# Optimization experiments

Measured on AMD Instinct MI355X. Metric: run time of the kernel, lower is better.

## Reference

```python
import jax, jax.numpy as jnp
import numpy as np

WS = 7   # window size
NH = 6   # num heads

def _ln(x, g, b, eps=1e-5):
    m = x.mean(-1, keepdims=True)
    v = jnp.var(x, axis=-1, keepdims=True)
    return (x - m) * jax.lax.rsqrt(v + eps) * g + b

def setup_inputs() -> dict:
    key = jax.random.key(0)
    ks = jax.random.split(key, 12)
    B, H, W, C = 32, 56, 56, 192
    hid = int(C * 2.0)
    def n(k, shape, s=0.02):
        return jax.random.normal(k, shape, jnp.float32) * s
    return {
        "x": jax.random.normal(ks[0], (B, H * W, C), jnp.float32),
        "H": H, "W": W,
        "ln1_g": jnp.ones((C,), jnp.float32), "ln1_b": jnp.zeros((C,), jnp.float32),
        "qkv_w": n(ks[1], (3 * C, C)), "qkv_b": jnp.zeros((3 * C,), jnp.float32),
        "proj_w": n(ks[2], (C, C)), "proj_b": jnp.zeros((C,), jnp.float32),
        "dw_w": n(ks[3], (C, 1, 3, 3)),          # depthwise 3x3, groups=C
        "pw_w": n(ks[4], (C, C)),                 # pointwise 1x1 conv (no bias)
        "gate_w": n(ks[5], (C, C)), "gate_b": jnp.zeros((C,), jnp.float32),
        "temp_w": n(ks[6], (C, C)), "temp_b": jnp.zeros((C,), jnp.float32),
        "spec_w": n(ks[7], (C, C)), "spec_b": jnp.zeros((C,), jnp.float32),
        "fuse_w": n(ks[8], (C, C)),                # fuse 1x1 conv (no bias)
        "ln2_g": jnp.ones((C,), jnp.float32), "ln2_b": jnp.zeros((C,), jnp.float32),
        "mlp1_w": n(ks[9], (hid, C)), "mlp1_b": jnp.zeros((hid,), jnp.float32),
        "mlp2_w": n(ks[10], (C, hid)), "mlp2_b": jnp.zeros((C,), jnp.float32),
    }

def reference(x, H, W, ln1_g, ln1_b, qkv_w, qkv_b, proj_w, proj_b, dw_w, pw_w,
              gate_w, gate_b, temp_w, temp_b, spec_w, spec_b, fuse_w,
              ln2_g, ln2_b, mlp1_w, mlp1_b, mlp2_w, mlp2_b):
    B, L, C = x.shape
    hd = C // NH
    scale = hd ** -0.5
    shortcut = x
    xn = _ln(x, ln1_g, ln1_b).reshape(B, H, W, C)
    # pad to multiple of window size (no-op when divisible)
    pad_b = (-H) % WS
    pad_r = (-W) % WS
    xp = jnp.pad(xn, ((0, 0), (0, pad_b), (0, pad_r), (0, 0)))
    Hp, Wp = H + pad_b, W + pad_r
    # window partition -> [B*nW, N, C]
    xw = xp.reshape(B, Hp // WS, WS, Wp // WS, WS, C).transpose(0, 1, 3, 2, 4, 5).reshape(-1, WS * WS, C)
    qkv = xw @ qkv_w.T + qkv_b
    q, k, v = [t.reshape(-1, WS * WS, NH, hd).transpose(0, 2, 1, 3) for t in jnp.split(qkv, 3, axis=-1)]
    attn = jax.nn.softmax(jnp.einsum('whnd,whmd->whnm', q * scale, k), axis=-1)
    aw = jnp.einsum('whnm,whmd->whnd', attn, v).transpose(0, 2, 1, 3).reshape(-1, WS * WS, C)
    aw = aw @ proj_w.T + proj_b
    # window reverse -> [B, Hp, Wp, C]
    xr = aw.reshape(B, Hp // WS, Wp // WS, WS, WS, C).transpose(0, 1, 3, 2, 4, 5).reshape(B, Hp, Wp, C)
    x_attn = xr[:, :H, :W, :].transpose(0, 3, 1, 2)     # [B,C,H,W]
    x_conv = xn.transpose(0, 3, 1, 2)                    # [B,C,H,W]
    # local_conv: depthwise 3x3 -> GELU -> pointwise 1x1
    ld = jax.lax.conv_general_dilated(x_conv, dw_w, (1, 1), 'SAME',
                                      feature_group_count=C,
                                      dimension_numbers=('NCHW', 'OIHW', 'NCHW'))
    ld = jnp.einsum('oc,bchw->bohw', pw_w, jax.nn.gelu(ld, approximate=False))
    # global gate: GAP -> linear -> sigmoid
    gate = jax.nn.sigmoid(x_conv.mean((2, 3)) @ gate_w.T + gate_b)[:, :, None, None]
    xf = x_attn + ld + x_conv * gate
    # spectral-temporal attention (outer product of two softmaxes, scale=2.0)
    a_t = jax.nn.softmax(jnp.einsum('oc,bcw->bow', temp_w, xf.mean(2)) + temp_b[None, :, None], axis=-1)
    a_s = jax.nn.softmax(jnp.einsum('oc,bch->boh', spec_w, xf.mean(3)) + spec_b[None, :, None], axis=-1)
    xf = xf * (a_s[:, :, :, None] * a_t[:, :, None, :]) * 2.0
    xf = jnp.einsum('oc,bchw->bohw', fuse_w, xf)         # fuse 1x1 conv
    x = shortcut + xf.transpose(0, 2, 3, 1).reshape(B, H * W, C)
    # MLP with pre-norm residual (1x1 conv expand == linear, then fc)
    h = _ln(x, ln2_g, ln2_b)
    h = jax.nn.gelu(h @ mlp1_w.T + mlp1_b, approximate=False)
    x = x + (h @ mlp2_w.T + mlp2_b)
    return x
```

## Files before the change

### kernel.cpp

```cpp
#include <hip/hip_runtime.h>
#include <hip/hip_bf16.h>

typedef __hip_bfloat16 bf16;

#define BB 32
#define HH 56
#define WW 56
#define CC 192
#define LL 3136
#define MM (BB*LL)
#define C3 576
#define HIDN 384
#define NHEAD 6
#define HD 32
#define NWIN 2048

typedef short short8 __attribute__((ext_vector_type(8)));
typedef float f32x4 __attribute__((ext_vector_type(4)));

__device__ __forceinline__ float us2f(unsigned short u) {
    union { unsigned int i; float f; } v; v.i = ((unsigned int)u) << 16; return v.f;
}
__device__ __forceinline__ float b2f(bf16 h) { return __bfloat162float(h); }
__device__ __forceinline__ bf16 f2b(float f) { return __float2bfloat16(f); }
__device__ __forceinline__ short f2bs(float f) { bf16 h = f2b(f); return *reinterpret_cast<short*>(&h); }
__device__ __forceinline__ unsigned pk2(float a, float b) {
    return (unsigned)(unsigned short)f2bs(a) | ((unsigned)(unsigned short)f2bs(b) << 16);
}
__device__ __forceinline__ float ldv(const bf16* p) { return b2f(*p); }
__device__ __forceinline__ float ldv(const float* p) { return *p; }
__device__ __forceinline__ void stv(bf16* p, float v) { *p = f2b(v); }
__device__ __forceinline__ void stv(float* p, float v) { *p = v; }
__device__ __forceinline__ float gelu_exact(float x) {
    return 0.5f * x * (1.0f + erff(x * 0.70710678118654752f));
}
__device__ __forceinline__ void async_lds16(const void* g, void* l) {
    __builtin_amdgcn_global_load_lds(
        (const __attribute__((address_space(1))) void*)g,
        (__attribute__((address_space(3))) void*)l, 16, 0, 0);
}

__global__ __launch_bounds__(256)
void cvt8_kernel(const float* __restrict__ s0, bf16* __restrict__ d0, int n0,
                 const float* __restrict__ s1, bf16* __restrict__ d1, int n1,
                 const float* __restrict__ s2, bf16* __restrict__ d2, int n2,
                 const float* __restrict__ s3, bf16* __restrict__ d3, int n3,
                 const float* __restrict__ s4, bf16* __restrict__ d4, int n4,
                 const float* __restrict__ s5, bf16* __restrict__ d5, int n5,
                 const float* __restrict__ s6, bf16* __restrict__ d6, int n6,
                 const float* __restrict__ s7, bf16* __restrict__ d7, int n7)
{
    int i = blockIdx.x * 256 + threadIdx.x;
    if (i < n0) { d0[i] = f2b(s0[i]); return; } i -= n0;
    if (i < n1) { d1[i] = f2b(s1[i]); return; } i -= n1;
    if (i < n2) { d2[i] = f2b(s2[i]); return; } i -= n2;
    if (i < n3) { d3[i] = f2b(s3[i]); return; } i -= n3;
    if (i < n4) { d4[i] = f2b(s4[i]); return; } i -= n4;
    if (i < n5) { d5[i] = f2b(s5[i]); return; } i -= n5;
    if (i < n6) { d6[i] = f2b(s6[i]); return; } i -= n6;
    if (i < n7) { d7[i] = f2b(s7[i]); }
}

template<typename IT>
__global__ __launch_bounds__(256)
void ln_kernel(const IT* __restrict__ in, const float* __restrict__ g,
               const float* __restrict__ bvec, bf16* __restrict__ out,
               bf16* __restrict__ xcopy)
{
    int wid = threadIdx.x >> 6, lane = threadIdx.x & 63;
    int row = blockIdx.x * 4 + wid;
    const IT* p = in + (size_t)row * CC;
    float x0 = ldv(p + lane);
    float x1 = ldv(p + lane + 64);
    float x2 = ldv(p + lane + 128);
    float s  = x0 + x1 + x2;
    float sq = x0*x0 + x1*x1 + x2*x2;
    #pragma unroll
    for (int o = 32; o > 0; o >>= 1) {
        s  += __shfl_xor(s,  o, 64);
        sq += __shfl_xor(sq, o, 64);
    }
    float mean = s * (1.0f / CC);
    float var  = sq * (1.0f / CC) - mean * mean;
    float inv  = rsqrtf(fmaxf(var, 0.0f) + 1e-5f);
    bf16* q = out + (size_t)row * CC;
    q[lane]       = f2b((x0 - mean) * inv * g[lane]       + bvec[lane]);
    q[lane + 64]  = f2b((x1 - mean) * inv * g[lane + 64]  + bvec[lane + 64]);
    q[lane + 128] = f2b((x2 - mean) * inv * g[lane + 128] + bvec[lane + 128]);
    if (xcopy) {
        bf16* xq = xcopy + (size_t)row * CC;
        xq[lane]       = f2b(x0);
        xq[lane + 64]  = f2b(x1);
        xq[lane + 128] = f2b(x2);
    }
}

template<int EPI, bool RESID, int NN, int KK, typename RT, typename OT>
__global__ __launch_bounds__(256)
void mfma_gemm(const bf16* __restrict__ A, const bf16* __restrict__ W,
               const float* __restrict__ bias, const RT* __restrict__ resid,
               OT* __restrict__ out,
               const bf16* __restrict__ xn2, const float* __restrict__ gate)
{
    __shared__ __align__(16) short Smem[128 * 64 + 64 * 64];
    short* As = Smem;
    short* Bs = Smem + 128 * 64;
    const int t    = threadIdx.x;
    const int lane = t & 63;
    const int w    = t >> 6;
    const int nx   = gridDim.x;
    const int nwg  = gridDim.x * gridDim.y;
    int hw  = blockIdx.y * nx + blockIdx.x;
    int wid = (nwg & 7) ? hw : ((hw & 7) * (nwg >> 3) + (hw >> 3));
    const int m0   = (wid / nx) * 128;
    const int n0   = (wid % nx) * 64;
    const int lr   = lane & 15;
    const int lg   = lane >> 4;

    f32x4 acc[2][4];
    #pragma unroll
    for (int i = 0; i < 2; ++i)
        #pragma unroll
        for (int j = 0; j < 4; ++j)
            acc[i][j] = (f32x4){0.f, 0.f, 0.f, 0.f};

    for (int k0 = 0; k0 < KK; k0 += 64) {
        const bf16* Ab = A + (size_t)m0 * KK + k0;
        const bf16* Wb = W + (size_t)n0 * KK + k0;
        #pragma unroll
        for (int li = 0; li < 4; ++li) {
            int chunk = li * 256 + t;
            int r = chunk >> 3, c = chunk & 7;
            int cs = c ^ (r & 7);
            async_lds16(Ab + (size_t)r * KK + (cs << 3),
                        &As[(li * 256 + w * 64) << 3]);
        }
        #pragma unroll
        for (int li = 0; li < 2; ++li) {
            int chunk = li * 256 + t;
            int r = chunk >> 3, c = chunk & 7;
            int cs = c ^ (r & 7);
            async_lds16(Wb + (size_t)r * KK + (cs << 3),
                        &Bs[(li * 256 + w * 64) << 3]);
        }
        __syncthreads();
        #pragma unroll
        for (int kf = 0; kf < 2; ++kf) {
            short8 a_[2], b_[4];
            #pragma unroll
            for (int mi = 0; mi < 2; ++mi) {
                int row = (w << 5) + (mi << 4) + lr;
                a_[mi] = *reinterpret_cast<const short8*>(
                    &As[(row << 6) + ((((kf << 2) + lg) ^ (row & 7)) << 3)]);
            }
            #pragma unroll
            for (int ni = 0; ni < 4; ++ni) {
                int rn = (ni << 4) + lr;
                b_[ni] = *reinterpret_cast<const short8*>(
                    &Bs[(rn << 6) + ((((kf << 2) + lg) ^ (rn & 7)) << 3)]);
            }
            #pragma unroll
            for (int mi = 0; mi < 2; ++mi)
                #pragma unroll
                for (int ni = 0; ni < 4; ++ni)
                    acc[mi][ni] = __builtin_amdgcn_mfma_f32_16x16x32_bf16(
                        a_[mi], b_[ni], acc[mi][ni], 0, 0, 0);
        }
        __syncthreads();
    }

    if constexpr (sizeof(OT) == 2) {
        short* cs = Smem + w * 3072;
        #pragma unroll
        for (int mi = 0; mi < 2; ++mi) {
            #pragma unroll
            for (int ni = 0; ni < 4; ++ni) {
                int col = n0 + (ni << 4) + lr;
                float bv = bias ? bias[col] : 0.f;
                #pragma unroll
                for (int r = 0; r < 4; ++r) {
                    int row = m0 + (w << 5) + (mi << 4) + (lg << 2) + r;
                    float c = acc[mi][ni][r] + bv;
                    if (EPI == 1) c = gelu_exact(c);
                    if (EPI == 2) {
                        int bidx = row / LL;
                        c += ldv(resid + (size_t)row * NN + col)
                           + b2f(xn2[(size_t)row * NN + col]) * gate[bidx * CC + col];
                    }
                    if (RESID) c += ldv(resid + (size_t)row * NN + col);
                    cs[((mi << 4) + (lg << 2) + r) * 72 + (ni << 4) + lr] = f2bs(c);
                }
            }
        }
        #pragma unroll
        for (int pass = 0; pass < 4; ++pass) {
            int r8 = (lane >> 3) + (pass << 3);
            int c8 = lane & 7;
            uint4 v = *reinterpret_cast<const uint4*>(&cs[r8 * 72 + (c8 << 3)]);
            *reinterpret_cast<uint4*>((bf16*)out + (size_t)(m0 + (w << 5) + r8) * NN
                                      + n0 + (c8 << 3)) = v;
        }
    } else {
        #pragma unroll
        for (int mi = 0; mi < 2; ++mi) {
            #pragma unroll
            for (int ni = 0; ni < 4; ++ni) {
                int col = n0 + (ni << 4) + lr;
                float bv = bias ? bias[col] : 0.f;
                #pragma unroll
                for (int r = 0; r < 4; ++r) {
                    int row = m0 + (w << 5) + (mi << 4) + (lg << 2) + r;
                    float c = acc[mi][ni][r] + bv;
                    if (EPI == 1) c = gelu_exact(c);
                    if (EPI == 2) {
                        int bidx = row / LL;
                        c += ldv(resid + (size_t)row * NN + col)
                           + b2f(xn2[(size_t)row * NN + col]) * gate[bidx * CC + col];
                    }
                    if (RESID) c += ldv(resid + (size_t)row * NN + col);
                    stv(out + (size_t)row * NN + col, c);
                }
            }
        }
    }
}

__global__ __launch_bounds__(256)
void winattn_kernel(const bf16* __restrict__ qkv, bf16* __restrict__ aw)
{
    __shared__ __align__(16) short Buf[4][2560];

    const int w  = threadIdx.x >> 6;
    const int t  = threadIdx.x & 63;
    const int p  = blockIdx.x * 4 + w;
    const int wi = p / 6;
    const int head = p - wi * 6;
    const int b  = wi >> 6;
    const int wr = wi & 63;
    const int wy = wr >> 3, wx = wr & 7;
    const int lc = t & 15;
    const int lg = t >> 4;
    const float scale = 0.1767766952966369f;
    const bf16* qbase = qkv + (size_t)b * LL * C3 + head * HD;
    short* buf = Buf[w];

    #pragma unroll
    for (int e = t; e < 512; e += 64) {
        int d = e >> 4, k = 48 + (e & 15);
        buf[(d << 6) + (((k >> 3) ^ (d & 7)) << 3) + (k & 7)] = 0;
    }
    for (int e = t; e < 196; e += 64) {
        int tok = e >> 2, part = e & 3;
        int iy = tok / 7, ix = tok - iy * 7;
        size_t l = (size_t)(wy * 7 + iy) * 56 + wx * 7 + ix;
        uint4 pv = *reinterpret_cast<const uint4*>(qbase + l * C3 + 384 + (part << 3));
        unsigned short uv[8];
        *reinterpret_cast<uint4*>(uv) = pv;
        #pragma unroll
        for (int jj = 0; jj < 8; ++jj) {
            int d = (part << 3) + jj;
            buf[(d << 6) + (((tok >> 3) ^ (d & 7)) << 3) + (tok & 7)] = (short)uv[jj];
        }
    }

    const short8 zero8 = {0, 0, 0, 0, 0, 0, 0, 0};
    short8 ka[4], qb[4];
    #pragma unroll
    for (int mi = 0; mi < 4; ++mi) {
        int key = (mi << 4) + lc;
        ka[mi] = zero8;
        if (key < 49) {
            int iy = key / 7, ix = key - iy * 7;
            size_t l = (size_t)(wy * 7 + iy) * 56 + wx * 7 + ix;
            ka[mi] = *reinterpret_cast<const short8*>(qbase + l * C3 + 192 + (lg << 3));
        }
    }
    #pragma unroll
    for (int nj = 0; nj < 4; ++nj) {
        int tok = (nj << 4) + lc;
        qb[nj] = zero8;
        if (tok < 49) {
            int iy = tok / 7, ix = tok - iy * 7;
            size_t l = (size_t)(wy * 7 + iy) * 56 + wx * 7 + ix;
            qb[nj] = *reinterpret_cast<const short8*>(qbase + l * C3 + (lg << 3));
        }
    }

    f32x4 acc[4][4];
    #pragma unroll
    for (int i = 0; i < 4; ++i)
        #pragma unroll
        for (int j = 0; j < 4; ++j)
            acc[i][j] = (f32x4){0.f, 0.f, 0.f, 0.f};
    #pragma unroll
    for (int mi = 0; mi < 4; ++mi)
        #pragma unroll
        for (int nj = 0; nj < 4; ++nj)
            acc[mi][nj] = __builtin_amdgcn_mfma_f32_16x16x32_bf16(
                ka[mi], qb[nj], acc[mi][nj], 0, 0, 0);

    float rinv[4];
    #pragma unroll
    for (int nj = 0; nj < 4; ++nj) {
        float mx = acc[0][nj][0];
        #pragma unroll
        for (int mi = 0; mi < 3; ++mi)
            #pragma unroll
            for (int r = 0; r < 4; ++r)
                mx = fmaxf(mx, acc[mi][nj][r]);
        float v48 = (lg == 0) ? acc[3][nj][0] : -1e30f;
        mx = fmaxf(mx, v48);
        mx = fmaxf(mx, __shfl_xor(mx, 16, 64));
        mx = fmaxf(mx, __shfl_xor(mx, 32, 64));
        float sm = 0.f;
        #pragma unroll
        for (int mi = 0; mi < 3; ++mi)
            #pragma unroll
            for (int r = 0; r < 4; ++r) {
                float e = __expf(scale * (acc[mi][nj][r] - mx));
                acc[mi][nj][r] = e;
                sm += e;
            }
        float e48 = (lg == 0) ? __expf(scale * (acc[3][nj][0] - mx)) : 0.f;
        acc[3][nj][0] = e48; sm += e48;
        acc[3][nj][1] = 0.f; acc[3][nj][2] = 0.f; acc[3][nj][3] = 0.f;
        sm += __shfl_xor(sm, 16, 64);
        sm += __shfl_xor(sm, 32, 64);
        rinv[nj] = 1.0f / sm;
    }

    f32x4 acc2[2][4];
    #pragma unroll
    for (int i = 0; i < 2; ++i)
        #pragma unroll
        for (int j = 0; j < 4; ++j)
            acc2[i][j] = (f32x4){0.f, 0.f, 0.f, 0.f};
    const int src0 = ((lg & 1) << 5) + lc;
    const int src1 = src0 + 16;
    const bool hi = (lg >> 1) != 0;
    #pragma unroll
    for (int kf = 0; kf < 2; ++kf) {
        short8 av[2];
        #pragma unroll
        for (int mi2 = 0; mi2 < 2; ++mi2) {
            int d = (mi2 << 4) + lc;
            av[mi2] = *reinterpret_cast<const short8*>(
                &buf[(d << 6) + ((((kf << 2) + lg) ^ (d & 7)) << 3)]);
        }
        #pragma unroll
        for (int nj = 0; nj < 4; ++nj) {
            unsigned A0 = pk2(acc[2*kf][nj][0],   acc[2*kf][nj][1]);
            unsigned A1 = pk2(acc[2*kf][nj][2],   acc[2*kf][nj][3]);
            unsigned B0 = pk2(acc[2*kf+1][nj][0], acc[2*kf+1][nj][1]);
            unsigned B1 = pk2(acc[2*kf+1][nj][2], acc[2*kf+1][nj][3]);
            unsigned xa0 = __shfl(A0, src0, 64), xa1 = __shfl(A1, src0, 64);
            unsigned xa2 = __shfl(A0, src1, 64), xa3 = __shfl(A1, src1, 64);
            unsigned xb0 = __shfl(B0, src0, 64), xb1 = __shfl(B1, src0, 64);
            unsigned xb2 = __shfl(B0, src1, 64), xb3 = __shfl(B1, src1, 64);
            union { unsigned u[4]; short8 s; } ub;
            ub.u[0] = hi ? xb0 : xa0;
            ub.u[1] = hi ? xb1 : xa1;
            ub.u[2] = hi ? xb2 : xa2;
            ub.u[3] = hi ? xb3 : xa3;
            #pragma unroll
            for (int mi2 = 0; mi2 < 2; ++mi2)
                acc2[mi2][nj] = __builtin_amdgcn_mfma_f32_16x16x32_bf16(
                    av[mi2], ub.s, acc2[mi2][nj], 0, 0, 0);
        }
    }

    #pragma unroll
    for (int mi2 = 0; mi2 < 2; ++mi2)
        #pragma unroll
        for (int nj = 0; nj < 4; ++nj) {
            int tokrow = (nj << 4) + lc;
            #pragma unroll
            for (int r = 0; r < 4; ++r) {
                int d = (mi2 << 4) + (lg << 2) + r;
                buf[tokrow * 40 + d] = f2bs(acc2[mi2][nj][r] * rinv[nj]);
            }
        }
    for (int e = t; e < 196; e += 64) {
        int tok = e >> 2, part = e & 3;
        int iy = tok / 7, ix = tok - iy * 7;
        size_t l = (size_t)(wy * 7 + iy) * 56 + wx * 7 + ix;
        *reinterpret_cast<uint4*>(aw + ((size_t)b * LL + l) * CC + head * HD + (part << 3)) =
            *reinterpret_cast<const uint4*>(&buf[tok * 40 + (part << 3)]);
    }
}

__global__ __launch_bounds__(256)
void dwconv_kernel(const bf16* __restrict__ xn, const float* __restrict__ w,
                   bf16* __restrict__ out)
{
    __shared__ float wl[9 * 288];
    const int t = threadIdx.x;
    for (int i = t; i < CC * 9; i += 256) {
        int c = i / 9, k = i - c * 9;
        wl[k * 288 + (c >> 3) * 12 + (c & 7)] = w[i];
    }
    __syncthreads();
    int e = blockIdx.x * 256 + t;
    int cg = e % 24;
    int pix = e / 24;
    int w_ = pix % WW;
    int t2 = pix / WW;
    int h_ = t2 % HH;
    int b  = t2 / HH;
    float acc[8] = {0.f,0.f,0.f,0.f,0.f,0.f,0.f,0.f};
    const bf16* rowbase = xn + ((size_t)b * HH * WW) * CC + (size_t)cg * 8;
    #pragma unroll
    for (int ky = 0; ky < 3; ++ky) {
        int hy = h_ + ky - 1;
        if (hy < 0 || hy >= HH) continue;
        #pragma unroll
        for (int kx = 0; kx < 3; ++kx) {
            int wx_ = w_ + kx - 1;
            if (wx_ < 0 || wx_ >= WW) continue;
            int k = ky * 3 + kx;
            const float4* wp = reinterpret_cast<const float4*>(&wl[k * 288 + cg * 12]);
            float4 w0 = wp[0];
            float4 w1 = wp[1];
            unsigned short u[8];
            *reinterpret_cast<uint4*>(u) = *reinterpret_cast<const uint4*>(
                rowbase + ((size_t)hy * WW + wx_) * CC);
            acc[0] += us2f(u[0]) * w0.x;
            acc[1] += us2f(u[1]) * w0.y;
            acc[2] += us2f(u[2]) * w0.z;
            acc[3] += us2f(u[3]) * w0.w;
            acc[4] += us2f(u[4]) * w1.x;
            acc[5] += us2f(u[5]) * w1.y;
            acc[6] += us2f(u[6]) * w1.z;
            acc[7] += us2f(u[7]) * w1.w;
        }
    }
    bf16 o8[8];
    #pragma unroll
    for (int j = 0; j < 8; ++j) o8[j] = f2b(gelu_exact(acc[j]));
    *reinterpret_cast<uint4*>(out + (size_t)e * 8) = *reinterpret_cast<uint4*>(o8);
}

__global__ __launch_bounds__(192)
void colsum_kernel(const bf16* __restrict__ xn, float* __restrict__ colsum)
{
    int b = blockIdx.y, g = blockIdx.x, c = threadIdx.x;
    float acc = 0.f;
    int l0 = g * 196;
    for (int l = l0; l < l0 + 196; ++l)
        acc += b2f(xn[((size_t)b * LL + l) * CC + c]);
    atomicAdd(&colsum[b * CC + c], acc);
}

__global__ __launch_bounds__(192)
void gate_kernel(const float* __restrict__ colsum, const float* __restrict__ gw,
                 const float* __restrict__ gb, float* __restrict__ gate)
{
    __shared__ float cm[CC];
    int b = blockIdx.x, o = threadIdx.x;
    cm[o] = colsum[b * CC + o] * (1.0f / LL);
    __syncthreads();
    float acc = gb[o];
    for (int c = 0; c < CC; ++c) acc += gw[o * CC + c] * cm[c];
    gate[b * CC + o] = 1.0f / (1.0f + expf(-acc));
}

__global__ __launch_bounds__(256)
void means_kernel(const bf16* __restrict__ xf, bf16* __restrict__ mh,
                  bf16* __restrict__ mw)
{
    int e = blockIdx.x * 256 + threadIdx.x;
    const int NHALF = BB * WW * 24;
    if (e < NHALF) {
        int cg = e % 24, c0 = cg << 3;
        int w_ = (e / 24) % WW;
        int b  = e / (24 * WW);
        float s[8] = {0.f,0.f,0.f,0.f,0.f,0.f,0.f,0.f};
        const bf16* base = xf + ((size_t)b * HH * WW + w_) * CC + c0;
        for (int h_ = 0; h_ < HH; ++h_) {
            unsigned short u[8];
            *reinterpret_cast<uint4*>(u) = *reinterpret_cast<const uint4*>(base + (size_t)h_ * WW * CC);
            #pragma unroll
            for (int j = 0; j < 8; ++j) s[j] += us2f(u[j]);
        }
        bf16 o8[8];
        #pragma unroll
        for (int j = 0; j < 8; ++j) o8[j] = f2b(s[j] * (1.0f / HH));
        *reinterpret_cast<uint4*>(mh + ((size_t)b * WW + w_) * CC + c0) =
            *reinterpret_cast<uint4*>(o8);
    } else {
        e -= NHALF;
        int cg = e % 24, c0 = cg << 3;
        int h_ = (e / 24) % HH;
        int b  = e / (24 * HH);
        float s[8] = {0.f,0.f,0.f,0.f,0.f,0.f,0.f,0.f};
        const bf16* base = xf + ((size_t)b * HH + h_) * WW * CC + c0;
        for (int w_ = 0; w_ < WW; ++w_) {
            unsigned short u[8];
            *reinterpret_cast<uint4*>(u) = *reinterpret_cast<const uint4*>(base + (size_t)w_ * CC);
            #pragma unroll
            for (int j = 0; j < 8; ++j) s[j] += us2f(u[j]);
        }
        bf16 o8[8];
        #pragma unroll
        for (int j = 0; j < 8; ++j) o8[j] = f2b(s[j] * (1.0f / WW));
        *reinterpret_cast<uint4*>(mw + ((size_t)b * HH + h_) * CC + c0) =
            *reinterpret_cast<uint4*>(o8);
    }
}

__global__ __launch_bounds__(256)
void axmfma_kernel(const bf16* __restrict__ mh, const bf16* __restrict__ wt,
                   float* __restrict__ at,
                   const bf16* __restrict__ mw, const bf16* __restrict__ ws,
                   float* __restrict__ as_)
{
    const int b = blockIdx.x;
    const bf16* mean; const bf16* wmat; float* out;
    if (blockIdx.y == 0) { mean = mh; wmat = wt; out = at; }
    else                 { mean = mw; wmat = ws; out = as_; }
    const int w  = threadIdx.x >> 6;
    const int t  = threadIdx.x & 63;
    const int lc = t & 15, lg = t >> 4;
    const bf16* mb = mean + (size_t)b * 56 * CC;
    const short8 zero8 = {0, 0, 0, 0, 0, 0, 0, 0};

    f32x4 acc[3][4];
    #pragma unroll
    for (int i = 0; i < 3; ++i)
        #pragma unroll
        for (int j = 0; j < 4; ++j)
            acc[i][j] = (f32x4){0.f, 0.f, 0.f, 0.f};

    #pragma unroll
    for (int kf = 0; kf < 6; ++kf) {
        short8 a_[3], b_[4];
        #pragma unroll
        for (int mi = 0; mi < 3; ++mi) {
            int o = ((w * 3 + mi) << 4) + lc;
            a_[mi] = *reinterpret_cast<const short8*>(wmat + (size_t)o * CC + (kf << 5) + (lg << 3));
        }
        #pragma unroll
        for (int ni = 0; ni < 4; ++ni) {
            int pos = (ni << 4) + lc;
            b_[ni] = (pos < 56)
                ? *reinterpret_cast<const short8*>(mb + (size_t)pos * CC + (kf << 5) + (lg << 3))
                : zero8;
        }
        #pragma unroll
        for (int mi = 0; mi < 3; ++mi)
            #pragma unroll
            for (int ni = 0; ni < 4; ++ni)
                acc[mi][ni] = __builtin_amdgcn_mfma_f32_16x16x32_bf16(
                    a_[mi], b_[ni], acc[mi][ni], 0, 0, 0);
    }

    #pragma unroll
    for (int mi = 0; mi < 3; ++mi) {
        #pragma unroll
        for (int r = 0; r < 4; ++r) {
            float mx = -1e30f;
            #pragma unroll
            for (int ni = 0; ni < 4; ++ni) {
                float v = acc[mi][ni][r];
                if (ni == 3 && lc >= 8) v = -1e30f;
                mx = fmaxf(mx, v);
            }
            mx = fmaxf(mx, __shfl_xor(mx, 1, 64));
            mx = fmaxf(mx, __shfl_xor(mx, 2, 64));
            mx = fmaxf(mx, __shfl_xor(mx, 4, 64));
            mx = fmaxf(mx, __shfl_xor(mx, 8, 64));
            float e[4];
            float sm = 0.f;
            #pragma unroll
            for (int ni = 0; ni < 4; ++ni) {
                e[ni] = (ni == 3 && lc >= 8) ? 0.f : __expf(acc[mi][ni][r] - mx);
                sm += e[ni];
            }
            sm += __shfl_xor(sm, 1, 64);
            sm += __shfl_xor(sm, 2, 64);
            sm += __shfl_xor(sm, 4, 64);
            sm += __shfl_xor(sm, 8, 64);
            float inv = 1.0f / sm;
            int o = ((w * 3 + mi) << 4) + (lg << 2) + r;
            #pragma unroll
            for (int ni = 0; ni < 4; ++ni) {
                int pos = (ni << 4) + lc;
                if (pos < 56)
                    out[((size_t)b * 56 + pos) * CC + o] = e[ni] * inv;
            }
        }
    }
}

__global__ __launch_bounds__(256)
void modulate_kernel(const bf16* __restrict__ xf, const float* __restrict__ a_s,
                     const float* __restrict__ a_t, bf16* __restrict__ xf2)
{
    int e = blockIdx.x * 256 + threadIdx.x;
    int cg = e % 24, c0 = cg << 3;
    int pix = e / 24;
    int w_ = pix % WW;
    int t2 = pix / WW;
    int h_ = t2 % HH;
    int b  = t2 / HH;
    unsigned short u[8];
    size_t base = (size_t)e * 8;
    *reinterpret_cast<uint4*>(u) = *reinterpret_cast<const uint4*>(xf + base);
    const float4* sp = reinterpret_cast<const float4*>(a_s + ((size_t)b * 56 + h_) * CC + c0);
    const float4* tp = reinterpret_cast<const float4*>(a_t + ((size_t)b * 56 + w_) * CC + c0);
    float4 s0 = sp[0], s1 = sp[1];
    float4 t0 = tp[0], t1 = tp[1];
    float ss[8] = {s0.x, s0.y, s0.z, s0.w, s1.x, s1.y, s1.z, s1.w};
    float tt[8] = {t0.x, t0.y, t0.z, t0.w, t1.x, t1.y, t1.z, t1.w};
    bf16 o8[8];
    #pragma unroll
    for (int j = 0; j < 8; ++j)
        o8[j] = f2b(us2f(u[j]) * ss[j] * tt[j] * 2.0f);
    *reinterpret_cast<uint4*>(xf2 + base) = *reinterpret_cast<uint4*>(o8);
}

extern "C" void kernel_launch(void* const* d_in, const int* in_sizes, int n_in,
                              void* d_out, int out_size, void* d_ws, size_t ws_size,
                              hipStream_t stream)
{
    const float* x      = (const float*)d_in[0];
    const float* ln1_g  = (const float*)d_in[3];
    const float* ln1_b  = (const float*)d_in[4];
    const float* qkv_w  = (const float*)d_in[5];
    const float* qkv_b  = (const float*)d_in[6];
    const float* proj_w = (const float*)d_in[7];
    const float* proj_b = (const float*)d_in[8];
    const float* dw_w   = (const float*)d_in[9];
    const float* pw_w   = (const float*)d_in[10];
    const float* gate_w = (const float*)d_in[11];
    const float* gate_b = (const float*)d_in[12];
    const float* temp_w = (const float*)d_in[13];
    const float* spec_w = (const float*)d_in[15];
    const float* fuse_w = (const float*)d_in[17];
    const float* ln2_g  = (const float*)d_in[18];
    const float* ln2_b  = (const float*)d_in[19];
    const float* mlp1_w = (const float*)d_in[20];
    const float* mlp1_b = (const float*)d_in[21];
    const float* mlp2_w = (const float*)d_in[22];
    const float* mlp2_b = (const float*)d_in[23];
    float* out = (float*)d_out;

    const size_t SLOT = (size_t)MM * CC * sizeof(bf16);
    char* ws = (char*)d_ws;

    bf16* s_xn    = (bf16*)(ws);
    bf16* s_qkv   = (bf16*)(ws + SLOT);
    bf16* s_aw    = (bf16*)(ws + 4 * SLOT);
    bf16* s_xattn = (bf16*)(ws + SLOT);
    bf16* s_dwg   = (bf16*)(ws + 2 * SLOT);
    bf16* s_xf    = (bf16*)(ws + 4 * SLOT);
    bf16* s_xf2   = (bf16*)(ws + 3 * SLOT);
    bf16* s_x2    = (bf16*)(ws);
    bf16* s_hn    = (bf16*)(ws + 2 * SLOT);
    bf16* s_h1    = (bf16*)(ws + 3 * SLOT);

    float* colsum  = (float*)(ws + 5 * SLOT);
    float* gatebuf = colsum + BB * CC;
    bf16*  mean_h  = (bf16*)(gatebuf + BB * CC);
    bf16*  mean_w  = mean_h + (size_t)BB * 56 * CC;
    float* a_t     = (float*)(mean_w + (size_t)BB * 56 * CC);
    float* a_s     = a_t + (size_t)BB * CC * 56;
    bf16* wb_qkv  = (bf16*)(a_s + (size_t)BB * CC * 56);
    bf16* wb_proj = wb_qkv  + C3 * CC;
    bf16* wb_pw   = wb_proj + CC * CC;
    bf16* wb_fuse = wb_pw   + CC * CC;
    bf16* wb_mlp1 = wb_fuse + CC * CC;
    bf16* wb_mlp2 = wb_mlp1 + HIDN * CC;
    bf16* wb_temp = wb_mlp2 + CC * HIDN;
    bf16* wb_spec = wb_temp + CC * CC;
    char* after_w = (char*)(wb_spec + CC * CC);
    size_t total_need = after_w - ws;
    if (ws_size < total_need) return;
    bf16* s_xb = (bf16*)after_w;
    bool have_xb = (ws_size >= total_need + SLOT);

    const int VEC_BLOCKS = MM * 24 / 256;
    const int CVT_N0 = C3 * CC, CVT_N1 = CC * CC, CVT_N4 = HIDN * CC;
    const int CVT_TOTAL = CVT_N0 + 5 * CVT_N1 + 2 * CVT_N4;

    cvt8_kernel<<<(CVT_TOTAL + 255) / 256, 256, 0, stream>>>(
        qkv_w, wb_qkv, CVT_N0, proj_w, wb_proj, CVT_N1, pw_w, wb_pw, CVT_N1,
        fuse_w, wb_fuse, CVT_N1, mlp1_w, wb_mlp1, CVT_N4, mlp2_w, wb_mlp2, CVT_N4,
        temp_w, wb_temp, CVT_N1, spec_w, wb_spec, CVT_N1);

    ln_kernel<float><<<MM / 4, 256, 0, stream>>>(x, ln1_g, ln1_b, s_xn,
                                                 have_xb ? s_xb : nullptr);
    mfma_gemm<0, false, C3, CC, bf16, bf16><<<dim3(C3 / 64, MM / 128), 256, 0, stream>>>(
        s_xn, wb_qkv, qkv_b, (const bf16*)nullptr, s_qkv, nullptr, nullptr);
    winattn_kernel<<<NWIN * NHEAD / 4, 256, 0, stream>>>(s_qkv, s_aw);
    mfma_gemm<0, false, CC, CC, bf16, bf16><<<dim3(CC / 64, MM / 128), 256, 0, stream>>>(
        s_aw, wb_proj, proj_b, (const bf16*)nullptr, s_xattn, nullptr, nullptr);
    dwconv_kernel<<<VEC_BLOCKS, 256, 0, stream>>>(s_xn, dw_w, s_dwg);
    hipMemsetAsync(colsum, 0, BB * CC * sizeof(float), stream);
    colsum_kernel<<<dim3(16, BB), 192, 0, stream>>>(s_xn, colsum);
    gate_kernel<<<BB, 192, 0, stream>>>(colsum, gate_w, gate_b, gatebuf);
    mfma_gemm<2, false, CC, CC, bf16, bf16><<<dim3(CC / 64, MM / 128), 256, 0, stream>>>(
        s_dwg, wb_pw, (const float*)nullptr, s_xattn, s_xf, s_xn, gatebuf);
    means_kernel<<<(2 * BB * WW * 24) / 256, 256, 0, stream>>>(s_xf, mean_h, mean_w);
    axmfma_kernel<<<dim3(BB, 2), 256, 0, stream>>>(
        mean_h, wb_temp, a_t, mean_w, wb_spec, a_s);
    modulate_kernel<<<VEC_BLOCKS, 256, 0, stream>>>(s_xf, a_s, a_t, s_xf2);
    if (have_xb)
        mfma_gemm<0, true, CC, CC, bf16, bf16><<<dim3(CC / 64, MM / 128), 256, 0, stream>>>(
            s_xf2, wb_fuse, (const float*)nullptr, s_xb, s_x2, nullptr, nullptr);
    else
        mfma_gemm<0, true, CC, CC, float, bf16><<<dim3(CC / 64, MM / 128), 256, 0, stream>>>(
            s_xf2, wb_fuse, (const float*)nullptr, x, s_x2, nullptr, nullptr);
    ln_kernel<bf16><<<MM / 4, 256, 0, stream>>>(s_x2, ln2_g, ln2_b, s_hn, nullptr);
    mfma_gemm<1, false, HIDN, CC, bf16, bf16><<<dim3(HIDN / 64, MM / 128), 256, 0, stream>>>(
        s_hn, wb_mlp1, mlp1_b, (const bf16*)nullptr, s_h1, nullptr, nullptr);
    mfma_gemm<0, true, CC, HIDN, bf16, float><<<dim3(CC / 64, MM / 128), 256, 0, stream>>>(
        s_h1, wb_mlp2, mlp2_b, s_x2, out, nullptr, nullptr);
}
```

Baseline: 368.0 us.

## Fuse QKV projection into window attention kernel, dropping qkv intermediate

Replaces the separate QKV GEMM and per-head window attention kernel with a single kernel per window that loads the 49 normalized tokens into LDS and computes Q, K and V for all six heads, one head per wavefront, using MFMA with register shuffles to form fragments. This removes writing and re-reading the large bf16 qkv tensor. In exchange each block reloads QKV weights from global/L2 and pads 49 tokens to 64, adding wasted MFMA work. Occupancy drops because of the larger block and LDS footprint.

```diff
diff --git a/kernel.cpp b/kernel.cpp
--- a/kernel.cpp
+++ b/kernel.cpp
@@ -38,6 +38,21 @@
     __builtin_amdgcn_global_load_lds(
         (const __attribute__((address_space(1))) void*)g,
         (__attribute__((address_space(3))) void*)l, 16, 0, 0);
+}
+__device__ __forceinline__ short8 cfrag(const f32x4& A, const f32x4& B,
+                                        int src0, int src1, bool hi) {
+    unsigned A0 = pk2(A[0], A[1]), A1 = pk2(A[2], A[3]);
+    unsigned B0 = pk2(B[0], B[1]), B1 = pk2(B[2], B[3]);
+    unsigned xa0 = __shfl(A0, src0, 64), xa1 = __shfl(A1, src0, 64);
+    unsigned xa2 = __shfl(A0, src1, 64), xa3 = __shfl(A1, src1, 64);
+    unsigned xb0 = __shfl(B0, src0, 64), xb1 = __shfl(B1, src0, 64);
+    unsigned xb2 = __shfl(B0, src1, 64), xb3 = __shfl(B1, src1, 64);
+    union { unsigned u[4]; short8 s; } ub;
+    ub.u[0] = hi ? xb0 : xa0;
+    ub.u[1] = hi ? xb1 : xa1;
+    ub.u[2] = hi ? xb2 : xa2;
+    ub.u[3] = hi ? xb3 : xa3;
+    return ub.s;
 }
 
 __global__ __launch_bounds__(256)
@@ -225,79 +240,170 @@
     }
 }
 
-__global__ __launch_bounds__(256)
-void winattn_kernel(const bf16* __restrict__ qkv, bf16* __restrict__ aw)
-{
-    __shared__ __align__(16) short Buf[4][2560];
-
-    const int w  = threadIdx.x >> 6;
-    const int t  = threadIdx.x & 63;
-    const int p  = blockIdx.x * 4 + w;
-    const int wi = p / 6;
-    const int head = p - wi * 6;
+__global__ __launch_bounds__(384)
+void qkvattn_kernel(const bf16* __restrict__ xn, const bf16* __restrict__ wqkv,
+                    const float* __restrict__ qbias, bf16* __restrict__ aw)
+{
+    __shared__ __align__(16) short Smem[64 * 192];
+
+    const int w    = threadIdx.x >> 6;
+    const int lane = threadIdx.x & 63;
+    const int wi   = blockIdx.x;
     const int b  = wi >> 6;
     const int wr = wi & 63;
     const int wy = wr >> 3, wx = wr & 7;
-    const int lc = t & 15;
-    const int lg = t >> 4;
+    const int lc = lane & 15;
+    const int lg = lane >> 4;
     const float scale = 0.1767766952966369f;
-    const bf16* qbase = qkv + (size_t)b * LL * C3 + head * HD;
-    short* buf = Buf[w];
-
-    #pragma unroll
-    for (int e = t; e < 512; e += 64) {
-        int d = e >> 4, k = 48 + (e & 15);
-        buf[(d << 6) + (((k >> 3) ^ (d & 7)) << 3) + (k & 7)] = 0;
-    }
-    for (int e = t; e < 196; e += 64) {
-        int tok = e >> 2, part = e & 3;
-        int iy = tok / 7, ix = tok - iy * 7;
-        size_t l = (size_t)(wy * 7 + iy) * 56 + wx * 7 + ix;
-        uint4 pv = *reinterpret_cast<const uint4*>(qbase + l * C3 + 384 + (part << 3));
-        unsigned short uv[8];
-        *reinterpret_cast<uint4*>(uv) = pv;
-        #pragma unroll
-        for (int jj = 0; jj < 8; ++jj) {
-            int d = (part << 3) + jj;
-            buf[(d << 6) + (((tok >> 3) ^ (d & 7)) << 3) + (tok & 7)] = (short)uv[jj];
-        }
-    }
-
-    const short8 zero8 = {0, 0, 0, 0, 0, 0, 0, 0};
-    short8 ka[4], qb[4];
-    #pragma unroll
-    for (int mi = 0; mi < 4; ++mi) {
-        int key = (mi << 4) + lc;
-        ka[mi] = zero8;
-        if (key < 49) {
-            int iy = key / 7, ix = key - iy * 7;
-            size_t l = (size_t)(wy * 7 + iy) * 56 + wx * 7 + ix;
-            ka[mi] = *reinterpret_cast<const short8*>(qbase + l * C3 + 192 + (lg << 3));
-        }
-    }
-    #pragma unroll
-    for (int nj = 0; nj < 4; ++nj) {
-        int tok = (nj << 4) + lc;
-        qb[nj] = zero8;
+    const bf16* xbase = xn + (size_t)b * LL * CC;
+
+    #pragma unroll
+    for (int li = 0; li < 4; ++li) {
+        int chunk = li * 384 + threadIdx.x;
+        int tok = chunk / 24, c = chunk - tok * 24;
         if (tok < 49) {
             int iy = tok / 7, ix = tok - iy * 7;
             size_t l = (size_t)(wy * 7 + iy) * 56 + wx * 7 + ix;
-            qb[nj] = *reinterpret_cast<const short8*>(qbase + l * C3 + (lg << 3));
-        }
+            int cs = (c & ~7) | ((c & 7) ^ (tok & 7));
+            async_lds16(xbase + l * CC + (cs << 3), &Smem[(li * 384 + w * 64) << 3]);
+        } else {
+            *reinterpret_cast<uint4*>(&Smem[chunk << 3]) = (uint4){0, 0, 0, 0};
+        }
+    }
+    __syncthreads();
+
+    const int src0 = ((lg & 1) << 5) + lc;
+    const int src1 = src0 + 16;
+    const bool hi = (lg >> 1) != 0;
+    const int qrow = w * HD;
+
+    short8 qb[4], ka[4], vfrag[2][2];
+    {
+        f32x4 aq[2][4];
+        #pragma unroll
+        for (int i = 0; i < 2; ++i)
+            #pragma unroll
+            for (int j = 0; j < 4; ++j)
+                aq[i][j] = (f32x4){0.f, 0.f, 0.f, 0.f};
+        #pragma unroll
+        for (int kf = 0; kf < 6; ++kf) {
+            short8 a0 = *reinterpret_cast<const short8*>(
+                wqkv + (size_t)(qrow + lc) * CC + (kf << 5) + (lg << 3));
+            short8 a1 = *reinterpret_cast<const short8*>(
+                wqkv + (size_t)(qrow + 16 + lc) * CC + (kf << 5) + (lg << 3));
+            #pragma unroll
+            for (int nj = 0; nj < 4; ++nj) {
+                int row = (nj << 4) + lc;
+                int cc = (kf << 2) + lg;
+                int cs = (cc & ~7) | ((cc & 7) ^ (row & 7));
+                short8 bx = *reinterpret_cast<const short8*>(&Smem[row * 192 + (cs << 3)]);
+                aq[0][nj] = __builtin_amdgcn_mfma_f32_16x16x32_bf16(a0, bx, aq[0][nj], 0, 0, 0);
+                aq[1][nj] = __builtin_amdgcn_mfma_f32_16x16x32_bf16(a1, bx, aq[1][nj], 0, 0, 0);
+            }
+        }
+        #pragma unroll
+        for (int mi = 0; mi < 2; ++mi) {
+            float bv = qbias[qrow + (mi << 4) + (lg << 2)];
+            float b1 = qbias[qrow + (mi << 4) + (lg << 2) + 1];
+            float b2 = qbias[qrow + (mi << 4) + (lg << 2) + 2];
+            float b3 = qbias[qrow + (mi << 4) + (lg << 2) + 3];
+            #pragma unroll
+            for (int nj = 0; nj < 4; ++nj) {
+                aq[mi][nj][0] += bv; aq[mi][nj][1] += b1;
+                aq[mi][nj][2] += b2; aq[mi][nj][3] += b3;
+            }
+        }
+        #pragma unroll
+        for (int nj = 0; nj < 4; ++nj)
+            qb[nj] = cfrag(aq[0][nj], aq[1][nj], src0, src1, hi);
+    }
+    {
+        f32x4 ak[2][4];
+        #pragma unroll
+        for (int i = 0; i < 2; ++i)
+            #pragma unroll
+            for (int j = 0; j < 4; ++j)
+                ak[i][j] = (f32x4){0.f, 0.f, 0.f, 0.f};
+        #pragma unroll
+        for (int kf = 0; kf < 6; ++kf) {
+            short8 a0 = *reinterpret_cast<const short8*>(
+                wqkv + (size_t)(CC + qrow + lc) * CC + (kf << 5) + (lg << 3));
+            short8 a1 = *reinterpret_cast<const short8*>(
+                wqkv + (size_t)(CC + qrow + 16 + lc) * CC + (kf << 5) + (lg << 3));
+            #pragma unroll
+            for (int nj = 0; nj < 4; ++nj) {
+                int row = (nj << 4) + lc;
+                int cc = (kf << 2) + lg;
+                int cs = (cc & ~7) | ((cc & 7) ^ (row & 7));
+                short8 bx = *reinterpret_cast<const short8*>(&Smem[row * 192 + (cs << 3)]);
+                ak[0][nj] = __builtin_amdgcn_mfma_f32_16x16x32_bf16(a0, bx, ak[0][nj], 0, 0, 0);
+                ak[1][nj] = __builtin_amdgcn_mfma_f32_16x16x32_bf16(a1, bx, ak[1][nj], 0, 0, 0);
+            }
+        }
+        #pragma unroll
+        for (int mi = 0; mi < 2; ++mi) {
+            float b0 = qbias[CC + qrow + (mi << 4) + (lg << 2)];
+            float b1 = qbias[CC + qrow + (mi << 4) + (lg << 2) + 1];
+            float b2 = qbias[CC + qrow + (mi << 4) + (lg << 2) + 2];
+            float b3 = qbias[CC + qrow + (mi << 4) + (lg << 2) + 3];
+            #pragma unroll
+            for (int nj = 0; nj < 4; ++nj) {
+                ak[mi][nj][0] += b0; ak[mi][nj][1] += b1;
+                ak[mi][nj][2] += b2; ak[mi][nj][3] += b3;
+            }
+        }
+        #pragma unroll
+        for (int nj = 0; nj < 4; ++nj)
+            ka[nj] = cfrag(ak[0][nj], ak[1][nj], src0, src1, hi);
+    }
+    {
+        f32x4 av[4][2];
+        #pragma unroll
+        for (int i = 0; i < 4; ++i)
+            #pragma unroll
+            for (int j = 0; j < 2; ++j)
+                av[i][j] = (f32x4){0.f, 0.f, 0.f, 0.f};
+        #pragma unroll
+        for (int kf = 0; kf < 6; ++kf) {
+            short8 bw[2];
+            #pragma unroll
+            for (int nj = 0; nj < 2; ++nj)
+                bw[nj] = *reinterpret_cast<const short8*>(
+                    wqkv + (size_t)(2 * CC + qrow + (nj << 4) + lc) * CC + (kf << 5) + (lg << 3));
+            #pragma unroll
+            for (int mi = 0; mi < 4; ++mi) {
+                int row = (mi << 4) + lc;
+                int cc = (kf << 2) + lg;
+                int cs = (cc & ~7) | ((cc & 7) ^ (row & 7));
+                short8 ax = *reinterpret_cast<const short8*>(&Smem[row * 192 + (cs << 3)]);
+                #pragma unroll
+                for (int nj = 0; nj < 2; ++nj)
+                    av[mi][nj] = __builtin_amdgcn_mfma_f32_16x16x32_bf16(ax, bw[nj], av[mi][nj], 0, 0, 0);
+            }
+        }
+        #pragma unroll
+        for (int nj = 0; nj < 2; ++nj) {
+            float bv = qbias[2 * CC + qrow + (nj << 4) + lc];
+            #pragma unroll
+            for (int mi = 0; mi < 4; ++mi) {
+                av[mi][nj][0] += bv; av[mi][nj][1] += bv;
+                av[mi][nj][2] += bv; av[mi][nj][3] += bv;
+            }
+        }
+        #pragma unroll
+        for (int kf = 0; kf < 2; ++kf)
+            #pragma unroll
+            for (int mi2 = 0; mi2 < 2; ++mi2)
+                vfrag[kf][mi2] = cfrag(av[2*kf][mi2], av[2*kf+1][mi2], src0, src1, hi);
     }
 
     f32x4 acc[4][4];
-    #pragma unroll
-    for (int i = 0; i < 4; ++i)
-        #pragma unroll
-        for (int j = 0; j < 4; ++j)
-            acc[i][j] = (f32x4){0.f, 0.f, 0.f, 0.f};
     #pragma unroll
     for (int mi = 0; mi < 4; ++mi)
         #pragma unroll
         for (int nj = 0; nj < 4; ++nj)
             acc[mi][nj] = __builtin_amdgcn_mfma_f32_16x16x32_bf16(
-                ka[mi], qb[nj], acc[mi][nj], 0, 0, 0);
+                ka[mi], qb[nj], (f32x4){0.f, 0.f, 0.f, 0.f}, 0, 0, 0);
 
     float rinv[4];
     #pragma unroll
@@ -329,63 +435,45 @@
         rinv[nj] = 1.0f / sm;
     }
 
-    f32x4 acc2[2][4];
+    f32x4 o2[2][4];
     #pragma unroll
     for (int i = 0; i < 2; ++i)
         #pragma unroll
         for (int j = 0; j < 4; ++j)
-            acc2[i][j] = (f32x4){0.f, 0.f, 0.f, 0.f};
-    const int src0 = ((lg & 1) << 5) + lc;
-    const int src1 = src0 + 16;
-    const bool hi = (lg >> 1) != 0;
+            o2[i][j] = (f32x4){0.f, 0.f, 0.f, 0.f};
     #pragma unroll
     for (int kf = 0; kf < 2; ++kf) {
-        short8 av[2];
-        #pragma unroll
-        for (int mi2 = 0; mi2 < 2; ++mi2) {
-            int d = (mi2 << 4) + lc;
-            av[mi2] = *reinterpret_cast<const short8*>(
-                &buf[(d << 6) + ((((kf << 2) + lg) ^ (d & 7)) << 3)]);
-        }
         #pragma unroll
         for (int nj = 0; nj < 4; ++nj) {
-            unsigned A0 = pk2(acc[2*kf][nj][0],   acc[2*kf][nj][1]);
-            unsigned A1 = pk2(acc[2*kf][nj][2],   acc[2*kf][nj][3]);
-            unsigned B0 = pk2(acc[2*kf+1][nj][0], acc[2*kf+1][nj][1]);
-            unsigned B1 = pk2(acc[2*kf+1][nj][2], acc[2*kf+1][nj][3]);
-            unsigned xa0 = __shfl(A0, src0, 64), xa1 = __shfl(A1, src0, 64);
-            unsigned xa2 = __shfl(A0, src1, 64), xa3 = __shfl(A1, src1, 64);
-            unsigned xb0 = __shfl(B0, src0, 64), xb1 = __shfl(B1, src0, 64);
-            unsigned xb2 = __shfl(B0, src1, 64), xb3 = __shfl(B1, src1, 64);
-            union { unsigned u[4]; short8 s; } ub;
-            ub.u[0] = hi ? xb0 : xa0;
-            ub.u[1] = hi ? xb1 : xa1;
-            ub.u[2] = hi ? xb2 : xa2;
-            ub.u[3] = hi ? xb3 : xa3;
+            short8 ub = cfrag(acc[2*kf][nj], acc[2*kf+1][nj], src0, src1, hi);
             #pragma unroll
             for (int mi2 = 0; mi2 < 2; ++mi2)
-                acc2[mi2][nj] = __builtin_amdgcn_mfma_f32_16x16x32_bf16(
-                    av[mi2], ub.s, acc2[mi2][nj], 0, 0, 0);
-        }
-    }
-
+                o2[mi2][nj] = __builtin_amdgcn_mfma_f32_16x16x32_bf16(
+                    vfrag[kf][mi2], ub, o2[mi2][nj], 0, 0, 0);
+        }
+    }
+
+    __syncthreads();
+    short* obuf = Smem + w * 2048;
     #pragma unroll
     for (int mi2 = 0; mi2 < 2; ++mi2)
         #pragma unroll
         for (int nj = 0; nj < 4; ++nj) {
-            int tokrow = (nj << 4) + lc;
-            #pragma unroll
-            for (int r = 0; r < 4; ++r) {
-                int d = (mi2 << 4) + (lg << 2) + r;
-                buf[tokrow * 40 + d] = f2bs(acc2[mi2][nj][r] * rinv[nj]);
-            }
-        }
-    for (int e = t; e < 196; e += 64) {
+            int tok = (nj << 4) + lc;
+            if (tok < 49) {
+                #pragma unroll
+                for (int r = 0; r < 4; ++r) {
+                    int d = (mi2 << 4) + (lg << 2) + r;
+                    obuf[tok * 40 + d] = f2bs(o2[mi2][nj][r] * rinv[nj]);
+                }
+            }
+        }
+    for (int e = lane; e < 196; e += 64) {
         int tok = e >> 2, part = e & 3;
         int iy = tok / 7, ix = tok - iy * 7;
         size_t l = (size_t)(wy * 7 + iy) * 56 + wx * 7 + ix;
-        *reinterpret_cast<uint4*>(aw + ((size_t)b * LL + l) * CC + head * HD + (part << 3)) =
-            *reinterpret_cast<const uint4*>(&buf[tok * 40 + (part << 3)]);
+        *reinterpret_cast<uint4*>(aw + ((size_t)b * LL + l) * CC + w * HD + (part << 3)) =
+            *reinterpret_cast<const uint4*>(&obuf[tok * 40 + (part << 3)]);
     }
 }
 
@@ -649,7 +737,6 @@
     char* ws = (char*)d_ws;
 
     bf16* s_xn    = (bf16*)(ws);
-    bf16* s_qkv   = (bf16*)(ws + SLOT);
     bf16* s_aw    = (bf16*)(ws + 4 * SLOT);
     bf16* s_xattn = (bf16*)(ws + SLOT);
     bf16* s_dwg   = (bf16*)(ws + 2 * SLOT);
@@ -690,9 +777,7 @@
 
     ln_kernel<float><<<MM / 4, 256, 0, stream>>>(x, ln1_g, ln1_b, s_xn,
                                                  have_xb ? s_xb : nullptr);
-    mfma_gemm<0, false, C3, CC, bf16, bf16><<<dim3(C3 / 64, MM / 128), 256, 0, stream>>>(
-        s_xn, wb_qkv, qkv_b, (const bf16*)nullptr, s_qkv, nullptr, nullptr);
-    winattn_kernel<<<NWIN * NHEAD / 4, 256, 0, stream>>>(s_qkv, s_aw);
+    qkvattn_kernel<<<NWIN, 384, 0, stream>>>(s_xn, wb_qkv, qkv_b, s_aw);
     mfma_gemm<0, false, CC, CC, bf16, bf16><<<dim3(CC / 64, MM / 128), 256, 0, stream>>>(
         s_aw, wb_proj, proj_b, (const bf16*)nullptr, s_xattn, nullptr, nullptr);
     dwconv_kernel<<<VEC_BLOCKS, 256, 0, stream>>>(s_xn, dw_w, s_dwg);
```

Result: slower. 409.8 us (+11.4%).

## Fuse attention projection GEMM into pointwise-conv GEMM via K-concatenation

Applied to the files above, without the earlier changes.

The proj GEMM over attention output and the pointwise-conv GEMM over the GELU'd depthwise output are merged into one GEMM with K=384. The A operand is read from two separate buffers, and the weights are packed side by side as [pw | proj]. This drops one launch plus the write and re-read of the x_attn intermediate (a full M×C bf16 tensor). The proj bias is now applied in the fused epilogue. The cost is a branch on the A pointer per k-tile.

```diff
diff --git a/kernel.cpp b/kernel.cpp
--- a/kernel.cpp
+++ b/kernel.cpp
@@ -46,9 +46,7 @@
                  const float* __restrict__ s2, bf16* __restrict__ d2, int n2,
                  const float* __restrict__ s3, bf16* __restrict__ d3, int n3,
                  const float* __restrict__ s4, bf16* __restrict__ d4, int n4,
-                 const float* __restrict__ s5, bf16* __restrict__ d5, int n5,
-                 const float* __restrict__ s6, bf16* __restrict__ d6, int n6,
-                 const float* __restrict__ s7, bf16* __restrict__ d7, int n7)
+                 const float* __restrict__ s5, bf16* __restrict__ d5, int n5)
 {
     int i = blockIdx.x * 256 + threadIdx.x;
     if (i < n0) { d0[i] = f2b(s0[i]); return; } i -= n0;
@@ -56,9 +54,23 @@
     if (i < n2) { d2[i] = f2b(s2[i]); return; } i -= n2;
     if (i < n3) { d3[i] = f2b(s3[i]); return; } i -= n3;
     if (i < n4) { d4[i] = f2b(s4[i]); return; } i -= n4;
-    if (i < n5) { d5[i] = f2b(s5[i]); return; } i -= n5;
-    if (i < n6) { d6[i] = f2b(s6[i]); return; } i -= n6;
-    if (i < n7) { d7[i] = f2b(s7[i]); }
+    if (i < n5) { d5[i] = f2b(s5[i]); }
+}
+
+__global__ __launch_bounds__(256)
+void cvtpack_kernel(const float* __restrict__ pw, const float* __restrict__ proj,
+                    bf16* __restrict__ cmb)
+{
+    int i = blockIdx.x * 256 + threadIdx.x;
+    int half = CC * CC;
+    if (i < half) {
+        int n = i / CC, k = i - n * CC;
+        cmb[(size_t)n * 384 + k] = f2b(pw[i]);
+    } else {
+        i -= half;
+        int n = i / CC, k = i - n * CC;
+        cmb[(size_t)n * 384 + 192 + k] = f2b(proj[i]);
+    }
 }
 
 template<typename IT>
@@ -95,9 +107,10 @@
     }
 }
 
-template<int EPI, bool RESID, int NN, int KK, typename RT, typename OT>
-__global__ __launch_bounds__(256)
-void mfma_gemm(const bf16* __restrict__ A, const bf16* __restrict__ W,
+template<int EPI, bool RESID, int NN, int KK, int KA, typename RT, typename OT>
+__global__ __launch_bounds__(256)
+void mfma_gemm(const bf16* __restrict__ A, const bf16* __restrict__ A2,
+               const bf16* __restrict__ W,
                const float* __restrict__ bias, const RT* __restrict__ resid,
                OT* __restrict__ out,
                const bf16* __restrict__ xn2, const float* __restrict__ gate)
@@ -125,14 +138,19 @@
             acc[i][j] = (f32x4){0.f, 0.f, 0.f, 0.f};
 
     for (int k0 = 0; k0 < KK; k0 += 64) {
-        const bf16* Ab = A + (size_t)m0 * KK + k0;
+        const bf16* Ab;
+        if constexpr (KA < KK)
+            Ab = (k0 < KA) ? A + (size_t)m0 * KA + k0
+                           : A2 + (size_t)m0 * KA + (k0 - KA);
+        else
+            Ab = A + (size_t)m0 * KA + k0;
         const bf16* Wb = W + (size_t)n0 * KK + k0;
         #pragma unroll
         for (int li = 0; li < 4; ++li) {
             int chunk = li * 256 + t;
             int r = chunk >> 3, c = chunk & 7;
             int cs = c ^ (r & 7);
-            async_lds16(Ab + (size_t)r * KK + (cs << 3),
+            async_lds16(Ab + (size_t)r * KA + (cs << 3),
                         &As[(li * 256 + w * 64) << 3]);
         }
         #pragma unroll
@@ -184,8 +202,7 @@
                     if (EPI == 1) c = gelu_exact(c);
                     if (EPI == 2) {
                         int bidx = row / LL;
-                        c += ldv(resid + (size_t)row * NN + col)
-                           + b2f(xn2[(size_t)row * NN + col]) * gate[bidx * CC + col];
+                        c += b2f(xn2[(size_t)row * NN + col]) * gate[bidx * CC + col];
                     }
                     if (RESID) c += ldv(resid + (size_t)row * NN + col);
                     cs[((mi << 4) + (lg << 2) + r) * 72 + (ni << 4) + lr] = f2bs(c);
@@ -214,8 +231,7 @@
                     if (EPI == 1) c = gelu_exact(c);
                     if (EPI == 2) {
                         int bidx = row / LL;
-                        c += ldv(resid + (size_t)row * NN + col)
-                           + b2f(xn2[(size_t)row * NN + col]) * gate[bidx * CC + col];
+                        c += b2f(xn2[(size_t)row * NN + col]) * gate[bidx * CC + col];
                     }
                     if (RESID) c += ldv(resid + (size_t)row * NN + col);
                     stv(out + (size_t)row * NN + col, c);
@@ -648,16 +664,15 @@
     const size_t SLOT = (size_t)MM * CC * sizeof(bf16);
     char* ws = (char*)d_ws;
 
-    bf16* s_xn    = (bf16*)(ws);
-    bf16* s_qkv   = (bf16*)(ws + SLOT);
-    bf16* s_aw    = (bf16*)(ws + 4 * SLOT);
-    bf16* s_xattn = (bf16*)(ws + SLOT);
-    bf16* s_dwg   = (bf16*)(ws + 2 * SLOT);
-    bf16* s_xf    = (bf16*)(ws + 4 * SLOT);
-    bf16* s_xf2   = (bf16*)(ws + 3 * SLOT);
-    bf16* s_x2    = (bf16*)(ws);
-    bf16* s_hn    = (bf16*)(ws + 2 * SLOT);
-    bf16* s_h1    = (bf16*)(ws + 3 * SLOT);
+    bf16* s_xn   = (bf16*)(ws);
+    bf16* s_qkv  = (bf16*)(ws + SLOT);
+    bf16* s_aw   = (bf16*)(ws + 4 * SLOT);
+    bf16* s_dwg  = (bf16*)(ws + 2 * SLOT);
+    bf16* s_xf   = (bf16*)(ws + 4 * SLOT);
+    bf16* s_xf2  = (bf16*)(ws + 3 * SLOT);
+    bf16* s_x2   = (bf16*)(ws);
+    bf16* s_hn   = (bf16*)(ws + 2 * SLOT);
+    bf16* s_h1   = (bf16*)(ws + 3 * SLOT);
 
     float* colsum  = (float*)(ws + 5 * SLOT);
     float* gatebuf = colsum + BB * CC;
@@ -666,9 +681,8 @@
     float* a_t     = (float*)(mean_w + (size_t)BB * 56 * CC);
     float* a_s     = a_t + (size_t)BB * CC * 56;
     bf16* wb_qkv  = (bf16*)(a_s + (size_t)BB * CC * 56);
-    bf16* wb_proj = wb_qkv  + C3 * CC;
-    bf16* wb_pw   = wb_proj + CC * CC;
-    bf16* wb_fuse = wb_pw   + CC * CC;
+    bf16* wb_cmb  = wb_qkv  + C3 * CC;
+    bf16* wb_fuse = wb_cmb  + CC * 2 * CC;
     bf16* wb_mlp1 = wb_fuse + CC * CC;
     bf16* wb_mlp2 = wb_mlp1 + HIDN * CC;
     bf16* wb_temp = wb_mlp2 + CC * HIDN;
@@ -681,39 +695,38 @@
 
     const int VEC_BLOCKS = MM * 24 / 256;
     const int CVT_N0 = C3 * CC, CVT_N1 = CC * CC, CVT_N4 = HIDN * CC;
-    const int CVT_TOTAL = CVT_N0 + 5 * CVT_N1 + 2 * CVT_N4;
+    const int CVT_TOTAL = CVT_N0 + 3 * CVT_N1 + 2 * CVT_N4;
 
     cvt8_kernel<<<(CVT_TOTAL + 255) / 256, 256, 0, stream>>>(
-        qkv_w, wb_qkv, CVT_N0, proj_w, wb_proj, CVT_N1, pw_w, wb_pw, CVT_N1,
-        fuse_w, wb_fuse, CVT_N1, mlp1_w, wb_mlp1, CVT_N4, mlp2_w, wb_mlp2, CVT_N4,
+        qkv_w, wb_qkv, CVT_N0, fuse_w, wb_fuse, CVT_N1,
+        mlp1_w, wb_mlp1, CVT_N4, mlp2_w, wb_mlp2, CVT_N4,
         temp_w, wb_temp, CVT_N1, spec_w, wb_spec, CVT_N1);
+    cvtpack_kernel<<<(2 * CC * CC + 255) / 256, 256, 0, stream>>>(pw_w, proj_w, wb_cmb);
 
     ln_kernel<float><<<MM / 4, 256, 0, stream>>>(x, ln1_g, ln1_b, s_xn,
                                                  have_xb ? s_xb : nullptr);
-    mfma_gemm<0, false, C3, CC, bf16, bf16><<<dim3(C3 / 64, MM / 128), 256, 0, stream>>>(
-        s_xn, wb_qkv, qkv_b, (const bf16*)nullptr, s_qkv, nullptr, nullptr);
+    mfma_gemm<0, false, C3, CC, CC, bf16, bf16><<<dim3(C3 / 64, MM / 128), 256, 0, stream>>>(
+        s_xn, nullptr, wb_qkv, qkv_b, (const bf16*)nullptr, s_qkv, nullptr, nullptr);
     winattn_kernel<<<NWIN * NHEAD / 4, 256, 0, stream>>>(s_qkv, s_aw);
-    mfma_gemm<0, false, CC, CC, bf16, bf16><<<dim3(CC / 64, MM / 128), 256, 0, stream>>>(
-        s_aw, wb_proj, proj_b, (const bf16*)nullptr, s_xattn, nullptr, nullptr);
     dwconv_kernel<<<VEC_BLOCKS, 256, 0, stream>>>(s_xn, dw_w, s_dwg);
     hipMemsetAsync(colsum, 0, BB * CC * sizeof(float), stream);
     colsum_kernel<<<dim3(16, BB), 192, 0, stream>>>(s_xn, colsum);
     gate_kernel<<<BB, 192, 0, stream>>>(colsum, gate_w, gate_b, gatebuf);
-    mfma_gemm<2, false, CC, CC, bf16, bf16><<<dim3(CC / 64, MM / 128), 256, 0, stream>>>(
-        s_dwg, wb_pw, (const float*)nullptr, s_xattn, s_xf, s_xn, gatebuf);
+    mfma_gemm<2, false, CC, 2 * CC, CC, bf16, bf16><<<dim3(CC / 64, MM / 128), 256, 0, stream>>>(
+        s_dwg, s_aw, wb_cmb, proj_b, (const bf16*)nullptr, s_xf, s_xn, gatebuf);
     means_kernel<<<(2 * BB * WW * 24) / 256, 256, 0, stream>>>(s_xf, mean_h, mean_w);
     axmfma_kernel<<<dim3(BB, 2), 256, 0, stream>>>(
         mean_h, wb_temp, a_t, mean_w, wb_spec, a_s);
     modulate_kernel<<<VEC_BLOCKS, 256, 0, stream>>>(s_xf, a_s, a_t, s_xf2);
     if (have_xb)
-        mfma_gemm<0, true, CC, CC, bf16, bf16><<<dim3(CC / 64, MM / 128), 256, 0, stream>>>(
-            s_xf2, wb_fuse, (const float*)nullptr, s_xb, s_x2, nullptr, nullptr);
+        mfma_gemm<0, true, CC, CC, CC, bf16, bf16><<<dim3(CC / 64, MM / 128), 256, 0, stream>>>(
+            s_xf2, nullptr, wb_fuse, (const float*)nullptr, s_xb, s_x2, nullptr, nullptr);
     else
-        mfma_gemm<0, true, CC, CC, float, bf16><<<dim3(CC / 64, MM / 128), 256, 0, stream>>>(
-            s_xf2, wb_fuse, (const float*)nullptr, x, s_x2, nullptr, nullptr);
+        mfma_gemm<0, true, CC, CC, CC, float, bf16><<<dim3(CC / 64, MM / 128), 256, 0, stream>>>(
+            s_xf2, nullptr, wb_fuse, (const float*)nullptr, x, s_x2, nullptr, nullptr);
     ln_kernel<bf16><<<MM / 4, 256, 0, stream>>>(s_x2, ln2_g, ln2_b, s_hn, nullptr);
-    mfma_gemm<1, false, HIDN, CC, bf16, bf16><<<dim3(HIDN / 64, MM / 128), 256, 0, stream>>>(
-        s_hn, wb_mlp1, mlp1_b, (const bf16*)nullptr, s_h1, nullptr, nullptr);
-    mfma_gemm<0, true, CC, HIDN, bf16, float><<<dim3(CC / 64, MM / 128), 256, 0, stream>>>(
-        s_h1, wb_mlp2, mlp2_b, s_x2, out, nullptr, nullptr);
-}
+    mfma_gemm<1, false, HIDN, CC, CC, bf16, bf16><<<dim3(HIDN / 64, MM / 128), 256, 0, stream>>>(
+        s_hn, nullptr, wb_mlp1, mlp1_b, (const bf16*)nullptr, s_h1, nullptr, nullptr);
+    mfma_gemm<0, true, CC, HIDN, HIDN, bf16, float><<<dim3(CC / 64, MM / 128), 256, 0, stream>>>(
+        s_h1, nullptr, wb_mlp2, mlp2_b, s_x2, out, nullptr, nullptr);
+}
```

Result: faster. 360.5 us, median of 2 (-2.0%).
